# Performance work log

Hardware: AMD Instinct MI355X
Metric: run time of the kernel (lower is better)

The kernel has to match this reference:

```python
import jax, jax.numpy as jnp
import numpy as np

N, D, S, K = 4096, 256, 32, 4   # nodes, in_dim(=out_dim), subspace_dim, num_heads
ETA = 0.5
LAMBDA_SPARSE = 0.05
EDGE_P = 0.02  # graph density for the random adjacency mask


def setup_inputs() -> dict:
    key = jax.random.key(0)
    k1, k2, k3 = jax.random.split(key, 3)
    H = jax.random.normal(k1, (N, D), dtype=jnp.float32)
    # binary adjacency mask with self-loops, stored as float (matches torch usage)
    mask = (jax.random.uniform(k2, (N, N)) < EDGE_P).astype(jnp.float32)
    adj_mask = jnp.maximum(mask, jnp.eye(N, dtype=jnp.float32))
    # per-head orthonormal subspace bases U[k] = qr(randn(D,S)) -> [K, D, S]
    raw = jax.random.normal(k3, (K, D, S), dtype=jnp.float32)
    U, _ = jnp.linalg.qr(raw)
    log_precision = jnp.zeros((K, S), dtype=jnp.float32)
    threshold = jnp.full((D,), LAMBDA_SPARSE, dtype=jnp.float32)
    return {"H": H, "adj_mask": adj_mask, "U": U,
            "log_precision": log_precision, "threshold": threshold}


def reference(H, adj_mask, U, log_precision, threshold):
    s = U.shape[-1]
    inv_sqrt_s = 1.0 / jnp.sqrt(jnp.asarray(s, dtype=H.dtype))
    neg = (1.0 - adj_mask) * (-1e9)  # [N, N] additive mask

    # scan over heads keeps peak memory at one [N,N] score matrix at a time
    def head_step(agg, xs):
        Uk, lpk = xs                       # [D,S], [S]
        Z = H @ Uk                         # [N,S]  (= Zk^T in the torch code)
        Zs = Z * jnp.exp(lpk)              # precision-scaled
        scores = (Zs @ Z.T) * inv_sqrt_s + neg   # [N,N]
        alpha = jax.nn.softmax(scores, axis=-1)
        agg = agg + (alpha @ Z) @ Uk.T     # [N,D] == (Uk @ (Zk @ alpha^T))^T
        return agg, None

    agg, _ = jax.lax.scan(head_step, jnp.zeros_like(H), (U, log_precision))
    H_half = H + ETA * agg                 # in_dim == out_dim -> no proj

    # soft threshold
    H_out = jnp.sign(H_half) * jax.nn.relu(jnp.abs(H_half) - threshold[None, :])

    # orthogonality loss: sum_k ||Uk^T Uk - I||_F^2 + sum_{k<l} ||Uk^T Ul||_F^2
    C = jnp.einsum('kda,ldb->klab', U, U)  # [K,K,S,S] gram blocks (K,S small)
    Kh = U.shape[0]
    I = jnp.eye(s, dtype=U.dtype)
    diag_blocks = C[jnp.arange(Kh), jnp.arange(Kh)]          # [K,S,S]
    orth_loss = ((diag_blocks - I) ** 2).sum()
    upper = jnp.triu(jnp.ones((Kh, Kh), dtype=U.dtype), 1)[:, :, None, None]
    orth_loss = orth_loss + ((C ** 2) * upper).sum()
    return H_out, orth_loss
```

## Files before the change

kernel.cpp:

```cpp
#include <hip/hip_runtime.h>
#include <math.h>

constexpr int NN = 4096;
constexpr int DD = 256;
constexpr int SS = 32;
constexpr int KK = 4;
constexpr int MAXN = 192;
constexpr int SEGMAX = 96;
constexpr float ETA = 0.5f;

#define MEMFENCE() __asm__ volatile("" ::: "memory")

__global__ __launch_bounds__(256) void prep_kernel(
    const float* __restrict__ H, const float* __restrict__ U,
    const float* __restrict__ lp, float* __restrict__ Z,
    float* __restrict__ elp, float* __restrict__ lossp) {
  __shared__ float Hl[16][DD];
  __shared__ float red[4];
  const int tid = threadIdx.x;

  if (blockIdx.x < 1024) {
    const int k = blockIdx.x & 3;
    const int n0 = (blockIdx.x >> 2) * 16;

    const float4* H4 = (const float4*)(H + (size_t)n0 * DD);
    float4* Hl4 = (float4*)&Hl[0][0];
    for (int i = tid; i < 16 * DD / 4; i += 256) Hl4[i] = H4[i];
    __syncthreads();

    const int s = tid & 31;
    const int n_l = (tid >> 5) & 7;
    const float* Uk = U + (size_t)k * DD * SS;
    float acc0 = 0.f, acc1 = 0.f;
#pragma unroll 4
    for (int dq = 0; dq < DD / 4; dq++) {
      const float4 h0 = Hl4[n_l * (DD / 4) + dq];
      const float4 h1 = Hl4[(n_l + 8) * (DD / 4) + dq];
      const float u0 = Uk[(4 * dq + 0) * SS + s];
      const float u1 = Uk[(4 * dq + 1) * SS + s];
      const float u2 = Uk[(4 * dq + 2) * SS + s];
      const float u3 = Uk[(4 * dq + 3) * SS + s];
      acc0 += h0.x * u0 + h0.y * u1 + h0.z * u2 + h0.w * u3;
      acc1 += h1.x * u0 + h1.y * u1 + h1.z * u2 + h1.w * u3;
    }
    Z[((size_t)k * NN + n0 + n_l) * SS + s] = acc0;
    Z[((size_t)k * NN + n0 + n_l + 8) * SS + s] = acc1;
  } else {
    const int pair = blockIdx.x - 1024;
    if (pair == 0 && tid < KK * SS) elp[tid] = expf(lp[tid]);
    const int pk[10] = {0, 0, 0, 0, 1, 1, 1, 2, 2, 3};
    const int pl[10] = {0, 1, 2, 3, 1, 2, 3, 2, 3, 3};
    const int k = pk[pair], l = pl[pair];
    const int b = tid & 31;
    const int a0 = tid >> 5;
    float acc[4] = {0.f, 0.f, 0.f, 0.f};
    for (int d = 0; d < DD; d++) {
      const float ub = U[((size_t)l * DD + d) * SS + b];
#pragma unroll
      for (int j = 0; j < 4; j++)
        acc[j] += U[((size_t)k * DD + d) * SS + a0 + 8 * j] * ub;
    }
    float tot = 0.f;
#pragma unroll
    for (int j = 0; j < 4; j++) {
      const float cv = acc[j] - ((k == l && (a0 + 8 * j) == b) ? 1.0f : 0.0f);
      tot += cv * cv;
    }
#pragma unroll
    for (int off = 32; off >= 1; off >>= 1) tot += __shfl_xor(tot, off);
    if ((tid & 63) == 0) red[tid >> 6] = tot;
    __syncthreads();
    if (tid == 0) lossp[pair] = red[0] + red[1] + red[2] + red[3];
  }
}

__global__ __launch_bounds__(256) void attn_row(
    const float* __restrict__ mask, const float* __restrict__ Z,
    const float* __restrict__ elp, const float* __restrict__ lossp,
    float* __restrict__ AO, float* __restrict__ loss) {
  const int tid = threadIdx.x;
  const int wv = tid >> 6;
  const int lane = tid & 63;
  const int row = blockIdx.x;

  __shared__ int segn[4][SEGMAX];
  __shared__ int segc[4];
  __shared__ int nbr[MAXN];
  __shared__ float scw[4][MAXN];

  if (blockIdx.x == 0 && tid == 0) {
    float t = 0.f;
#pragma unroll
    for (int i = 0; i < 10; i++) t += lossp[i];
    loss[0] = t;
  }

  const float4* m4 = (const float4*)(mask + (size_t)row * NN);
  const unsigned long long lt = (1ULL << lane) - 1ULL;
  int cnt = 0;
#pragma unroll
  for (int it = 0; it < 4; it++) {
    const int i = wv * 256 + it * 64 + lane;
    const float4 v = m4[i];
    unsigned long long b;
    b = __ballot(v.x > 0.5f);
    if (v.x > 0.5f) { const int p = cnt + (int)__popcll(b & lt); if (p < SEGMAX) segn[wv][p] = 4 * i; }
    cnt += (int)__popcll(b);
    b = __ballot(v.y > 0.5f);
    if (v.y > 0.5f) { const int p = cnt + (int)__popcll(b & lt); if (p < SEGMAX) segn[wv][p] = 4 * i + 1; }
    cnt += (int)__popcll(b);
    b = __ballot(v.z > 0.5f);
    if (v.z > 0.5f) { const int p = cnt + (int)__popcll(b & lt); if (p < SEGMAX) segn[wv][p] = 4 * i + 2; }
    cnt += (int)__popcll(b);
    b = __ballot(v.w > 0.5f);
    if (v.w > 0.5f) { const int p = cnt + (int)__popcll(b & lt); if (p < SEGMAX) segn[wv][p] = 4 * i + 3; }
    cnt += (int)__popcll(b);
  }
  if (lane == 0) segc[wv] = min(cnt, SEGMAX);
  MEMFENCE();
  __syncthreads();

  const int c0 = segc[0], c1 = segc[1], c2 = segc[2], c3 = segc[3];
  const int offs[4] = {0, c0, c0 + c1, c0 + c1 + c2};
  const int c = min(c0 + c1 + c2 + c3, MAXN);
  const int myc = segc[wv];
  const int myoff = offs[wv];
  for (int i = lane; i < myc; i += 64) {
    const int p = myoff + i;
    if (p < MAXN) nbr[p] = segn[wv][i];
  }
  MEMFENCE();
  __syncthreads();

  const int k = wv;
  const int p_sub = lane >> 3;
  const int sq = lane & 7;
  const float inv_sqrt_s = 0.17677669529663687f;
  const float* Zk = Z + (size_t)k * NN * SS;

  float4 q4;
  {
    const float4 a = ((const float4*)(Z + ((size_t)k * NN + row) * SS))[sq];
    const float4 e = ((const float4*)(elp + k * SS))[sq];
    q4.x = a.x * e.x; q4.y = a.y * e.y; q4.z = a.z * e.z; q4.w = a.w * e.w;
  }

  float lmax = -3.0e38f;
  for (int p0 = 0; p0 < c; p0 += 16) {
    const int pa = p0 + p_sub;
    const int pb = pa + 8;
    const bool aA = pa < c, aB = pb < c;
    float4 zA = {0.f, 0.f, 0.f, 0.f}, zB = {0.f, 0.f, 0.f, 0.f};
    if (aA) zA = ((const float4*)(Zk + (size_t)nbr[pa] * SS))[sq];
    if (aB) zB = ((const float4*)(Zk + (size_t)nbr[pb] * SS))[sq];
    float dA = q4.x * zA.x + q4.y * zA.y + q4.z * zA.z + q4.w * zA.w;
    float dB = q4.x * zB.x + q4.y * zB.y + q4.z * zB.z + q4.w * zB.w;
    dA += __shfl_xor(dA, 1); dB += __shfl_xor(dB, 1);
    dA += __shfl_xor(dA, 2); dB += __shfl_xor(dB, 2);
    dA += __shfl_xor(dA, 4); dB += __shfl_xor(dB, 4);
    dA = aA ? dA * inv_sqrt_s : -3.0e38f;
    dB = aB ? dB * inv_sqrt_s : -3.0e38f;
    if (sq == 0 && aA) scw[wv][pa] = dA;
    if (sq == 0 && aB) scw[wv][pb] = dB;
    lmax = fmaxf(lmax, fmaxf(dA, dB));
  }
  MEMFENCE();
#pragma unroll
  for (int off = 32; off >= 1; off >>= 1) lmax = fmaxf(lmax, __shfl_xor(lmax, off));

  float wsum = 0.f;
#pragma unroll
  for (int t = 0; t < 3; t++) {
    const int p = lane + t * 64;
    if (p < c) {
      const float w = __expf(scw[wv][p] - lmax);
      scw[wv][p] = w;
      wsum += w;
    }
  }
  MEMFENCE();
#pragma unroll
  for (int off = 32; off >= 1; off >>= 1) wsum += __shfl_xor(wsum, off);
  const float invl = 1.0f / wsum;

  float4 o4 = {0.f, 0.f, 0.f, 0.f};
  for (int p0 = 0; p0 < c; p0 += 16) {
    const int pa = p0 + p_sub;
    const int pb = pa + 8;
    const bool aA = pa < c, aB = pb < c;
    float wA = 0.f, wB = 0.f;
    float4 zA = {0.f, 0.f, 0.f, 0.f}, zB = {0.f, 0.f, 0.f, 0.f};
    if (aA) { wA = scw[wv][pa]; zA = ((const float4*)(Zk + (size_t)nbr[pa] * SS))[sq]; }
    if (aB) { wB = scw[wv][pb]; zB = ((const float4*)(Zk + (size_t)nbr[pb] * SS))[sq]; }
    o4.x += wA * zA.x + wB * zB.x;
    o4.y += wA * zA.y + wB * zB.y;
    o4.z += wA * zA.z + wB * zB.z;
    o4.w += wA * zA.w + wB * zB.w;
  }
#pragma unroll
  for (int off = 8; off <= 32; off <<= 1) {
    o4.x += __shfl_xor(o4.x, off);
    o4.y += __shfl_xor(o4.y, off);
    o4.z += __shfl_xor(o4.z, off);
    o4.w += __shfl_xor(o4.w, off);
  }
  if (p_sub == 0) {
    float4 o;
    o.x = o4.x * invl; o.y = o4.y * invl; o.z = o4.z * invl; o.w = o4.w * invl;
    ((float4*)AO)[(size_t)row * (KK * SS / 4) + k * 8 + sq] = o;
  }
}

__global__ __launch_bounds__(256) void epilogue_kernel(
    const float* __restrict__ H, const float* __restrict__ U,
    const float* __restrict__ thr, const float* __restrict__ AO,
    float* __restrict__ Hout) {
  __shared__ float AOl[4][KK * SS];
  const int tid = threadIdx.x;
  const int r0 = blockIdx.x * 4;

  const float4* AO4 = (const float4*)(AO + (size_t)r0 * KK * SS);
  float4* AOl4 = (float4*)&AOl[0][0];
  if (tid < 128) AOl4[tid] = AO4[tid];
  __syncthreads();

  const int d = tid;
  float acc[4] = {0.f, 0.f, 0.f, 0.f};
  const float4* U4 = (const float4*)U;
#pragma unroll
  for (int k = 0; k < KK; k++) {
    const int ubase = (k * DD + d) * (SS / 4);
#pragma unroll
    for (int sq = 0; sq < SS / 4; sq++) {
      const float4 u = U4[ubase + sq];
#pragma unroll
      for (int r = 0; r < 4; r++) {
        const float4 a = AOl4[r * (KK * SS / 4) + k * (SS / 4) + sq];
        acc[r] += u.x * a.x + u.y * a.y + u.z * a.z + u.w * a.w;
      }
    }
  }
  const float tv = thr[d];
#pragma unroll
  for (int r = 0; r < 4; r++) {
    const float h = H[(size_t)(r0 + r) * DD + d] + ETA * acc[r];
    const float ab = fabsf(h) - tv;
    Hout[(size_t)(r0 + r) * DD + d] = (ab > 0.0f) ? copysignf(ab, h) : 0.0f;
  }
}

extern "C" void kernel_launch(void* const* d_in, const int* in_sizes, int n_in,
                              void* d_out, int out_size, void* d_ws, size_t ws_size,
                              hipStream_t stream) {
  const float* H    = (const float*)d_in[0];
  const float* mask = (const float*)d_in[1];
  const float* U    = (const float*)d_in[2];
  const float* lp   = (const float*)d_in[3];
  const float* thr  = (const float*)d_in[4];

  float* Hout = (float*)d_out;
  float* loss = Hout + (size_t)NN * DD;

  float* Z     = (float*)d_ws;
  float* AO    = Z + (size_t)KK * NN * SS;
  float* elp   = AO + (size_t)NN * KK * SS;
  float* lossp = elp + KK * SS;

  prep_kernel<<<1034, 256, 0, stream>>>(H, U, lp, Z, elp, lossp);
  attn_row<<<NN, 256, 0, stream>>>(mask, Z, elp, lossp, AO, loss);
  epilogue_kernel<<<NN / 4, 256, 0, stream>>>(H, U, thr, AO, Hout);
}
```

Baseline: 164.4 us.

## Move adjacency mask compaction into prep kernel, overlapping with Z projection

Neighbor-list extraction from the dense mask moves out of the attention kernel into extra blocks of the prep kernel, one wave per row, writing compacted indices and counts to global workspace. The mask scan can now run concurrently with the Z projection blocks, and the attention kernel drops two block barriers and its shared segment buffers. In exchange, the attention kernel reads neighbor indices from global memory instead of LDS, and each row is scanned serially by a single wave rather than by four waves in parallel.

```diff
diff --git a/kernel.cpp b/kernel.cpp
--- a/kernel.cpp
+++ b/kernel.cpp
@@ -6,20 +6,19 @@
 constexpr int SS = 32;
 constexpr int KK = 4;
 constexpr int MAXN = 192;
-constexpr int SEGMAX = 96;
 constexpr float ETA = 0.5f;
 
 #define MEMFENCE() __asm__ volatile("" ::: "memory")
 
 __global__ __launch_bounds__(256) void prep_kernel(
     const float* __restrict__ H, const float* __restrict__ U,
-    const float* __restrict__ lp, float* __restrict__ Z,
-    float* __restrict__ elp, float* __restrict__ lossp) {
-  __shared__ float Hl[16][DD];
-  __shared__ float red[4];
+    const float* __restrict__ lp, const float* __restrict__ mask,
+    float* __restrict__ Z, float* __restrict__ elp, float* __restrict__ lossp,
+    int* __restrict__ nbr_g, int* __restrict__ cnt_g) {
   const int tid = threadIdx.x;
 
   if (blockIdx.x < 1024) {
+    __shared__ float Hl[16][DD];
     const int k = blockIdx.x & 3;
     const int n0 = (blockIdx.x >> 2) * 16;
 
@@ -45,8 +44,36 @@
     }
     Z[((size_t)k * NN + n0 + n_l) * SS + s] = acc0;
     Z[((size_t)k * NN + n0 + n_l + 8) * SS + s] = acc1;
+  } else if (blockIdx.x < 2048) {
+    const int wv = tid >> 6;
+    const int lane = tid & 63;
+    const int row = (blockIdx.x - 1024) * 4 + wv;
+    const float4* m4 = (const float4*)(mask + (size_t)row * NN);
+    const unsigned long long lt = (1ULL << lane) - 1ULL;
+    int* out = nbr_g + (size_t)row * MAXN;
+    int cnt = 0;
+#pragma unroll 4
+    for (int it = 0; it < 16; it++) {
+      const int i = it * 64 + lane;
+      const float4 v = m4[i];
+      unsigned long long b;
+      b = __ballot(v.x > 0.5f);
+      if (v.x > 0.5f) { const int p = cnt + (int)__popcll(b & lt); if (p < MAXN) out[p] = 4 * i; }
+      cnt += (int)__popcll(b);
+      b = __ballot(v.y > 0.5f);
+      if (v.y > 0.5f) { const int p = cnt + (int)__popcll(b & lt); if (p < MAXN) out[p] = 4 * i + 1; }
+      cnt += (int)__popcll(b);
+      b = __ballot(v.z > 0.5f);
+      if (v.z > 0.5f) { const int p = cnt + (int)__popcll(b & lt); if (p < MAXN) out[p] = 4 * i + 2; }
+      cnt += (int)__popcll(b);
+      b = __ballot(v.w > 0.5f);
+      if (v.w > 0.5f) { const int p = cnt + (int)__popcll(b & lt); if (p < MAXN) out[p] = 4 * i + 3; }
+      cnt += (int)__popcll(b);
+    }
+    if (lane == 0) cnt_g[row] = min(cnt, MAXN);
   } else {
-    const int pair = blockIdx.x - 1024;
+    __shared__ float red[4];
+    const int pair = blockIdx.x - 2048;
     if (pair == 0 && tid < KK * SS) elp[tid] = expf(lp[tid]);
     const int pk[10] = {0, 0, 0, 0, 1, 1, 1, 2, 2, 3};
     const int pl[10] = {0, 1, 2, 3, 1, 2, 3, 2, 3, 3};
@@ -75,17 +102,15 @@
 }
 
 __global__ __launch_bounds__(256) void attn_row(
-    const float* __restrict__ mask, const float* __restrict__ Z,
-    const float* __restrict__ elp, const float* __restrict__ lossp,
-    float* __restrict__ AO, float* __restrict__ loss) {
+    const float* __restrict__ Z, const float* __restrict__ elp,
+    const float* __restrict__ lossp, const int* __restrict__ nbr_g,
+    const int* __restrict__ cnt_g, float* __restrict__ AO,
+    float* __restrict__ loss) {
   const int tid = threadIdx.x;
   const int wv = tid >> 6;
   const int lane = tid & 63;
   const int row = blockIdx.x;
 
-  __shared__ int segn[4][SEGMAX];
-  __shared__ int segc[4];
-  __shared__ int nbr[MAXN];
   __shared__ float scw[4][MAXN];
 
   if (blockIdx.x == 0 && tid == 0) {
@@ -95,42 +120,8 @@
     loss[0] = t;
   }
 
-  const float4* m4 = (const float4*)(mask + (size_t)row * NN);
-  const unsigned long long lt = (1ULL << lane) - 1ULL;
-  int cnt = 0;
-#pragma unroll
-  for (int it = 0; it < 4; it++) {
-    const int i = wv * 256 + it * 64 + lane;
-    const float4 v = m4[i];
-    unsigned long long b;
-    b = __ballot(v.x > 0.5f);
-    if (v.x > 0.5f) { const int p = cnt + (int)__popcll(b & lt); if (p < SEGMAX) segn[wv][p] = 4 * i; }
-    cnt += (int)__popcll(b);
-    b = __ballot(v.y > 0.5f);
-    if (v.y > 0.5f) { const int p = cnt + (int)__popcll(b & lt); if (p < SEGMAX) segn[wv][p] = 4 * i + 1; }
-    cnt += (int)__popcll(b);
-    b = __ballot(v.z > 0.5f);
-    if (v.z > 0.5f) { const int p = cnt + (int)__popcll(b & lt); if (p < SEGMAX) segn[wv][p] = 4 * i + 2; }
-    cnt += (int)__popcll(b);
-    b = __ballot(v.w > 0.5f);
-    if (v.w > 0.5f) { const int p = cnt + (int)__popcll(b & lt); if (p < SEGMAX) segn[wv][p] = 4 * i + 3; }
-    cnt += (int)__popcll(b);
-  }
-  if (lane == 0) segc[wv] = min(cnt, SEGMAX);
-  MEMFENCE();
-  __syncthreads();
-
-  const int c0 = segc[0], c1 = segc[1], c2 = segc[2], c3 = segc[3];
-  const int offs[4] = {0, c0, c0 + c1, c0 + c1 + c2};
-  const int c = min(c0 + c1 + c2 + c3, MAXN);
-  const int myc = segc[wv];
-  const int myoff = offs[wv];
-  for (int i = lane; i < myc; i += 64) {
-    const int p = myoff + i;
-    if (p < MAXN) nbr[p] = segn[wv][i];
-  }
-  MEMFENCE();
-  __syncthreads();
+  const int c = cnt_g[row];
+  const int* nb = nbr_g + (size_t)row * MAXN;
 
   const int k = wv;
   const int p_sub = lane >> 3;
@@ -151,8 +142,8 @@
     const int pb = pa + 8;
     const bool aA = pa < c, aB = pb < c;
     float4 zA = {0.f, 0.f, 0.f, 0.f}, zB = {0.f, 0.f, 0.f, 0.f};
-    if (aA) zA = ((const float4*)(Zk + (size_t)nbr[pa] * SS))[sq];
-    if (aB) zB = ((const float4*)(Zk + (size_t)nbr[pb] * SS))[sq];
+    if (aA) zA = ((const float4*)(Zk + (size_t)nb[pa] * SS))[sq];
+    if (aB) zB = ((const float4*)(Zk + (size_t)nb[pb] * SS))[sq];
     float dA = q4.x * zA.x + q4.y * zA.y + q4.z * zA.z + q4.w * zA.w;
     float dB = q4.x * zB.x + q4.y * zB.y + q4.z * zB.z + q4.w * zB.w;
     dA += __shfl_xor(dA, 1); dB += __shfl_xor(dB, 1);
@@ -190,8 +181,8 @@
     const bool aA = pa < c, aB = pb < c;
     float wA = 0.f, wB = 0.f;
     float4 zA = {0.f, 0.f, 0.f, 0.f}, zB = {0.f, 0.f, 0.f, 0.f};
-    if (aA) { wA = scw[wv][pa]; zA = ((const float4*)(Zk + (size_t)nbr[pa] * SS))[sq]; }
-    if (aB) { wB = scw[wv][pb]; zB = ((const float4*)(Zk + (size_t)nbr[pb] * SS))[sq]; }
+    if (aA) { wA = scw[wv][pa]; zA = ((const float4*)(Zk + (size_t)nb[pa] * SS))[sq]; }
+    if (aB) { wB = scw[wv][pb]; zB = ((const float4*)(Zk + (size_t)nb[pb] * SS))[sq]; }
     o4.x += wA * zA.x + wB * zB.x;
     o4.y += wA * zA.y + wB * zB.y;
     o4.z += wA * zA.z + wB * zB.z;
@@ -265,8 +256,10 @@
   float* AO    = Z + (size_t)KK * NN * SS;
   float* elp   = AO + (size_t)NN * KK * SS;
   float* lossp = elp + KK * SS;
-
-  prep_kernel<<<1034, 256, 0, stream>>>(H, U, lp, Z, elp, lossp);
-  attn_row<<<NN, 256, 0, stream>>>(mask, Z, elp, lossp, AO, loss);
+  int*   nbr_g = (int*)(lossp + 16);
+  int*   cnt_g = nbr_g + (size_t)NN * MAXN;
+
+  prep_kernel<<<2058, 256, 0, stream>>>(H, U, lp, mask, Z, elp, lossp, nbr_g, cnt_g);
+  attn_row<<<NN, 256, 0, stream>>>(Z, elp, lossp, nbr_g, cnt_g, AO, loss);
   epilogue_kernel<<<NN / 4, 256, 0, stream>>>(H, U, thr, AO, Hout);
 }
```

Result: slower. 171.0 us (+4.0%).
